# Performance work log

Hardware: AMD Instinct MI355X
Metric: run time of the kernel (lower is better)

## Reference

```python
import jax, jax.numpy as jnp
import numpy as np

B, C, L, D, P = 64, 64, 720, 512, 336
P2, H = P // 2, 512  # H = hidden width of the ProbG branch


def setup_inputs() -> dict:
    key = jax.random.key(0)
    ks = jax.random.split(key, 20)
    def w(k, i, o):
        return jax.random.normal(k, (i, o), jnp.float32) / np.sqrt(i)
    return {
        "x_bsd": jax.random.normal(ks[0], (B, L, C), jnp.float32),
        "z0": jax.random.normal(ks[1], (B, C, D), jnp.float32),
        "y0": jax.random.normal(ks[2], (B, C, P), jnp.float32),
        # ProbG hidden branch (HID_GIVEN_X_V0 -> SS_Z_GIVEN_X_V0)
        "W_h": w(ks[3], L, H),
        "W_ssz": w(ks[4], H, 2 * D),
        # x->z scale/shift flows (versions v2..v5)
        "W_xz_v2": w(ks[5], L, 2 * D),
        "W_xz_v3": w(ks[6], L, 2 * D),
        "W_xz_v4": w(ks[7], L, 2 * D),
        "W_xz_v5": w(ks[8], L, 2 * D),
        # z->x scale/shift flows (v0, v2, v3, v5)
        "W_zx_v0": w(ks[9], D, 2 * L),
        "W_zx_v2": w(ks[10], D, 2 * L),
        "W_zx_v3": w(ks[11], D, 2 * L),
        "W_zx_v5": w(ks[12], D, 2 * L),
        # z->y scale/shift flow (v4, used inside encoding)
        "W_zy_v4": w(ks[13], D, 2 * P),
        # decode heads: ROT_IN_Y_V1 and KOO_Y_GIVEN_Z_V0
        "W_rot": w(ks[14], D, P2),
        "W_koo": w(ks[15], D, 2 * P),
        # Koopman complex params for y-space (a + i b per channel/pair)
        "a_y": jnp.ones((C, P2), jnp.float32),
        "b_y": jnp.zeros((C, P2), jnp.float32) + 0.1,
    }


def _ss(params):
    """Split conditioner output into (positive scale, shift)."""
    s_raw, t = jnp.split(params, 2, axis=-1)
    return jnp.exp(jnp.tanh(s_raw)), t


def _affine(v, cond, W):
    """Scale/shift flow: v <- v * s(cond) + t(cond)."""
    s, t = _ss(jnp.einsum('bck,km->bcm', cond, W))
    return v * s + t


def _rot(u, theta, inv=False):
    """Rotate interleaved (re, im) pairs of u [B,C,P] by angles theta [B,C,P/2]."""
    re, im = u[..., 0::2], u[..., 1::2]
    th = -theta if inv else theta
    c, s = jnp.cos(th), jnp.sin(th)
    return jnp.stack([c * re - s * im, s * re + c * im], axis=-1).reshape(u.shape)


def _koop(u, a, b, inv=False):
    """Koopman unit-complex multiply on interleaved pairs; a,b [C,P/2]."""
    n = jnp.sqrt(a * a + b * b)
    ca, cb = a / n, b / n
    cb = -cb if inv else cb
    re, im = u[..., 0::2], u[..., 1::2]
    return jnp.stack([ca * re - cb * im, cb * re + ca * im], axis=-1).reshape(u.shape)


def reference(x_bsd, z0, y0, W_h, W_ssz, W_xz_v2, W_xz_v3, W_xz_v4, W_xz_v5,
              W_zx_v0, W_zx_v2, W_zx_v3, W_zx_v5, W_zy_v4, W_rot, W_koo, a_y, b_y):
    x = jnp.transpose(x_bsd, (0, 2, 1))  # [B,C,L]
    z = z0 * 0.1                          # [B,C,D]
    y = y0 * 0.1                          # [B,C,P]
    # ---- encoding phase ----
    h = jax.nn.gelu(jnp.einsum('bcl,lk->bck', x, W_h))  # X_to_Z_PROB hidden
    z = _affine(z, h, W_ssz)
    x = _affine(x, z, W_zx_v0)
    z = _affine(z, x, W_xz_v2); x = _affine(x, z, W_zx_v2)
    z = _affine(z, x, W_xz_v3); x = _affine(x, z, W_zx_v3)
    z = _affine(z, x, W_xz_v4); y = _affine(y, z, W_zy_v4)  # Z_to_Y_V4
    z = _affine(z, x, W_xz_v5); x = _affine(x, z, W_zx_v5)
    pre_y = y
    # ---- decode: rotate -> ky -> scale -> ky.inv -> rot.inv -> shift ----
    theta = jnp.pi * jnp.tanh(jnp.einsum('bcd,dp->bcp', z, W_rot))   # [B,C,P/2]
    scale, shift = _ss(jnp.einsum('bcd,dp->bcp', z, W_koo))          # [B,C,P]
    const = _koop(_rot(pre_y, theta), a_y, b_y)
    accu = const * scale
    accu = _rot(_koop(accu, a_y, b_y, inv=True), theta, inv=True) + shift
    return jnp.transpose(accu, (0, 2, 1))  # [B,P,C]
```

## Files before the change

kernel.cpp:

```cpp
#include <hip/hip_runtime.h>
#include <hip/hip_bf16.h>
#include <math.h>

#define BB  64
#define CC  64
#define LL  720
#define LLP 736
#define DD  512
#define PP  336
#define P2C 168
#define HH  512
#define MM  (BB*CC)

typedef _Float16 f16x8 __attribute__((ext_vector_type(8)));
typedef float    f32x4 __attribute__((ext_vector_type(4)));

#define GLDS16(g, l) __builtin_amdgcn_global_load_lds( \
    (const __attribute__((address_space(1))) void*)(g), \
    (__attribute__((address_space(3))) void*)(l), 16, 0, 0)

__device__ __forceinline__ float ftanh(float x) {
  const float ax = fabsf(x);
  const float e  = __expf(2.f * ax);
  const float t  = 1.f - 2.f / (e + 1.f);
  return copysignf(t, x);
}

struct WDesc { const float* src; _Float16* dstHi; _Float16* dstLo;
               int K, N, Kpad, tbase, tilesN; };
struct WTab  { WDesc d[12]; };

__global__ __launch_bounds__(256) void k_convert(WTab tab) {
  __shared__ float tile[16][17];
  const int bid = blockIdx.x;
  int wi = 0;
#pragma unroll
  for (int i = 1; i < 12; ++i) if (bid >= tab.d[i].tbase) wi = i;
  const WDesc d = tab.d[wi];
  const int lt = bid - d.tbase;
  const int tk = lt / d.tilesN, tn = lt % d.tilesN;
  const int k0 = tk * 16, n0 = tn * 16;
  const int tx = threadIdx.x & 15, ty = threadIdx.x >> 4;
  float v = 0.f;
  if (n0 + tx < d.N) v = d.src[(size_t)(k0 + ty) * d.N + n0 + tx];
  tile[ty][tx] = v;
  __syncthreads();
  if (n0 + ty < d.N) {
    const float w = tile[tx][ty];
    const _Float16 h = (_Float16)w;
    const _Float16 l = (_Float16)(w - (float)h);
    const size_t base = (size_t)(n0 + ty) * d.Kpad;
    d.dstHi[base + k0 + tx] = h;
    d.dstLo[base + k0 + tx] = l;
    if (d.Kpad != d.K && k0 + 16 == d.K) {
      d.dstHi[base + d.K + tx] = (_Float16)0.f;
      d.dstLo[base + d.K + tx] = (_Float16)0.f;
    }
  }
}

__global__ __launch_bounds__(256) void k_xpose(const float* __restrict__ xbsd,
                                               _Float16* __restrict__ xhi,
                                               _Float16* __restrict__ xlo) {
  __shared__ float tile[16][17];
  const int b = blockIdx.z, l0 = blockIdx.x * 16, c0 = blockIdx.y * 16;
  const int tx = threadIdx.x, ty = threadIdx.y;
  tile[ty][tx] = xbsd[(size_t)b * LL * CC + (size_t)(l0 + ty) * CC + c0 + tx];
  __syncthreads();
  const float v = tile[tx][ty];
  const _Float16 h = (_Float16)v;
  const _Float16 l = (_Float16)(v - (float)h);
  const size_t m = (size_t)b * CC + c0 + ty;
  xhi[m * LLP + l0 + tx] = h;
  xlo[m * LLP + l0 + tx] = l;
  if (l0 == 704) {
    xhi[m * LLP + 720 + tx] = (_Float16)0.f;
    xlo[m * LLP + 720 + tx] = (_Float16)0.f;
  }
}

template<int EPI, bool DUAL, bool VIN16, bool OUT_T>
__global__ __launch_bounds__(256)
void k_gemm(const _Float16* Ahi, const _Float16* Alo, int lda,
            const _Float16* Whi, const _Float16* Wlo, int ldw,
            const float* Vin32, const _Float16* VinHi,
            const _Float16* VinLo, int ldv, float vscale,
            float* outT32,
            _Float16* outHi, _Float16* outLo, int ldo,
            int Kp, int Nv) {
  constexpr int NB   = DUAL ? 128 : 64;
  constexpr int ABUF = 64 * 32;
  constexpr int BBUF = NB * 32;
  constexpr int SBUF = 2 * ABUF + 2 * BBUF;
  constexpr int NCH  = 8 + 2 * (NB / 16);
  constexpr int NCHW = NCH / 4;
  __shared__ _Float16 smem[2 * SBUF];

  const int gx  = gridDim.x;
  const int nwg = gx * gridDim.y;
  const int id  = blockIdx.y * gx + blockIdx.x;
  const int nid = (id & 7) * (nwg >> 3) + (id >> 3);
  const int m0 = (nid / gx) * 64;
  const int n0 = (nid % gx) * 64;

  {
    const unsigned ph = ((unsigned)nid * 2654435761u) >> 29;
    for (unsigned i = 0; i < ph; ++i) __builtin_amdgcn_s_sleep(8);
  }

  const int tid = threadIdx.x;
  const int w = tid >> 6, lane = tid & 63, q = lane >> 4, r = lane & 15;
  const int wr = (w & 1) * 32, wc = (w >> 1) * 32;
  const int lr = lane >> 2, ls = lane & 3;

  f32x4 accS[2][2] = {};
  f32x4 accT[2][2] = {};

  auto stage = [&](int kc, int bsel) {
    const int k0 = kc << 5;
    _Float16* sb = smem + bsel * SBUF;
#pragma unroll
    for (int cc = 0; cc < NCHW; ++cc) {
      const int chunk = w * NCHW + cc;
      const _Float16* gsrc;
      _Float16* ldst;
      if (chunk < 4) {
        const int rb = chunk * 16;
        const int R = rb + lr;
        const int ss = ls ^ ((R >> 1) & 3);
        gsrc = Ahi + (size_t)(m0 + R) * lda + k0 + ss * 8;
        ldst = sb + rb * 32;
      } else if (chunk < 8) {
        const int rb = (chunk - 4) * 16;
        const int R = rb + lr;
        const int ss = ls ^ ((R >> 1) & 3);
        gsrc = Alo + (size_t)(m0 + R) * lda + k0 + ss * 8;
        ldst = sb + ABUF + rb * 32;
      } else if (chunk < 8 + NB / 16) {
        const int rb = (chunk - 8) * 16;
        const int R = rb + lr;
        const int ss = ls ^ ((R >> 1) & 3);
        const int wrow = (R < 64) ? (n0 + R) : (Nv + n0 + (R - 64));
        gsrc = Whi + (size_t)wrow * ldw + k0 + ss * 8;
        ldst = sb + 2 * ABUF + rb * 32;
      } else {
        const int rb = (chunk - 8 - NB / 16) * 16;
        const int R = rb + lr;
        const int ss = ls ^ ((R >> 1) & 3);
        const int wrow = (R < 64) ? (n0 + R) : (Nv + n0 + (R - 64));
        gsrc = Wlo + (size_t)wrow * ldw + k0 + ss * 8;
        ldst = sb + 2 * ABUF + BBUF + rb * 32;
      }
      GLDS16(gsrc, ldst);
    }
  };

  const int nk = Kp >> 5;
  stage(0, 0);
  int cur = 0;
  for (int kc = 0; kc < nk; ++kc) {
    __syncthreads();
    if (kc + 1 < nk) stage(kc + 1, cur ^ 1);
    const _Float16* sb = smem + cur * SBUF;

    f16x8 ah[2], al[2];
#pragma unroll
    for (int rt = 0; rt < 2; ++rt) {
      const int R = wr + rt * 16 + r;
      const int t = (q ^ ((R >> 1) & 3)) * 8;
      ah[rt] = *(const f16x8*)(sb + R * 32 + t);
      al[rt] = *(const f16x8*)(sb + ABUF + R * 32 + t);
    }
#pragma unroll
    for (int ct = 0; ct < 2; ++ct) {
      const int RB = wc + ct * 16 + r;
      const int tb = (q ^ ((RB >> 1) & 3)) * 8;
      const f16x8 bh = *(const f16x8*)(sb + 2 * ABUF + RB * 32 + tb);
      const f16x8 bl = *(const f16x8*)(sb + 2 * ABUF + BBUF + RB * 32 + tb);
#pragma unroll
      for (int rt = 0; rt < 2; ++rt) {
        accS[rt][ct] = __builtin_amdgcn_mfma_f32_16x16x32_f16(ah[rt], bh, accS[rt][ct], 0, 0, 0);
        accS[rt][ct] = __builtin_amdgcn_mfma_f32_16x16x32_f16(al[rt], bh, accS[rt][ct], 0, 0, 0);
        accS[rt][ct] = __builtin_amdgcn_mfma_f32_16x16x32_f16(ah[rt], bl, accS[rt][ct], 0, 0, 0);
      }
      if (DUAL) {
        const int RT = 64 + RB;
        const int tt = (q ^ ((RT >> 1) & 3)) * 8;
        const f16x8 chh = *(const f16x8*)(sb + 2 * ABUF + RT * 32 + tt);
        const f16x8 cll = *(const f16x8*)(sb + 2 * ABUF + BBUF + RT * 32 + tt);
#pragma unroll
        for (int rt = 0; rt < 2; ++rt) {
          accT[rt][ct] = __builtin_amdgcn_mfma_f32_16x16x32_f16(ah[rt], chh, accT[rt][ct], 0, 0, 0);
          accT[rt][ct] = __builtin_amdgcn_mfma_f32_16x16x32_f16(al[rt], chh, accT[rt][ct], 0, 0, 0);
          accT[rt][ct] = __builtin_amdgcn_mfma_f32_16x16x32_f16(ah[rt], cll, accT[rt][ct], 0, 0, 0);
        }
      }
    }
    cur ^= 1;
  }

#pragma unroll
  for (int rt = 0; rt < 2; ++rt) {
    const int mb = m0 + wr + rt * 16 + q * 4;
#pragma unroll
    for (int ct = 0; ct < 2; ++ct) {
      const int n = n0 + wc + ct * 16 + r;
      if (n >= Nv) continue;
      if (EPI == 2) {
        *(f32x4*)(outT32 + (size_t)n * MM + mb) = accS[rt][ct];
      } else if (EPI == 1) {
#pragma unroll
        for (int g = 0; g < 4; ++g) {
          const int m = mb + g;
          const float v = accS[rt][ct][g];
          const float o = 0.5f * v * (1.0f + ftanh(0.7978845608028654f * (v + 0.044715f * v * v * v)));
          const _Float16 h = (_Float16)o;
          outHi[(size_t)m * ldo + n] = h;
          outLo[(size_t)m * ldo + n] = (_Float16)(o - (float)h);
        }
      } else {
        f32x4 o;
#pragma unroll
        for (int g = 0; g < 4; ++g) {
          const int m = mb + g;
          float v;
          if (VIN16) {
            v = (float)VinHi[(size_t)m * ldv + n] + (float)VinLo[(size_t)m * ldv + n];
          } else {
            v = Vin32[(size_t)m * ldv + n];
          }
          const float s = __expf(ftanh(accS[rt][ct][g]));
          o[g] = v * vscale * s + accT[rt][ct][g];
        }
        if (OUT_T) {
          *(f32x4*)(outT32 + (size_t)n * MM + mb) = o;
        } else {
#pragma unroll
          for (int g = 0; g < 4; ++g) {
            const int m = mb + g;
            const _Float16 h = (_Float16)o[g];
            outHi[(size_t)m * ldo + n] = h;
            outLo[(size_t)m * ldo + n] = (_Float16)(o[g] - (float)h);
          }
        }
      }
    }
  }
}

__global__ __launch_bounds__(256) void k_final(const float* __restrict__ Pt,
                                               const float* __restrict__ yT,
                                               const float* __restrict__ Ay,
                                               const float* __restrict__ By,
                                               float* __restrict__ out) {
  const int c = threadIdx.x;
  const int j = blockIdx.x * 4 + threadIdx.y;
  const int b = blockIdx.y;
  const int m = b * 64 + c;
  const float th = 3.14159265358979323846f * ftanh(Pt[(size_t)j * MM + m]);
  const float sc0 = __expf(ftanh(Pt[(size_t)(168 + 2 * j) * MM + m]));
  const float sc1 = __expf(ftanh(Pt[(size_t)(169 + 2 * j) * MM + m]));
  const float t0 = Pt[(size_t)(504 + 2 * j) * MM + m];
  const float t1 = Pt[(size_t)(505 + 2 * j) * MM + m];
  const float re = yT[(size_t)(2 * j) * MM + m];
  const float im = yT[(size_t)(2 * j + 1) * MM + m];
  const float a = Ay[c * P2C + j], bb = By[c * P2C + j];
  const float rn = rsqrtf(a * a + bb * bb);
  const float ca = a * rn, cb = bb * rn;
  float s1v, c1;
  __sincosf(th, &s1v, &c1);
  const float r1 = c1 * re - s1v * im, i1 = s1v * re + c1 * im;
  const float r2 = ca * r1 - cb * i1,  i2 = cb * r1 + ca * i1;
  const float r3 = r2 * sc0,           i3 = i2 * sc1;
  const float r4 = ca * r3 + cb * i3,  i4 = ca * i3 - cb * r3;
  const float r5 = c1 * r4 + s1v * i4, i5 = c1 * i4 - s1v * r4;
  out[(size_t)b * PP * CC + (size_t)(2 * j) * CC + c]     = r5 + t0;
  out[(size_t)b * PP * CC + (size_t)(2 * j + 1) * CC + c] = i5 + t1;
}

extern "C" void kernel_launch(void* const* d_in, const int* in_sizes, int n_in,
                              void* d_out, int out_size, void* d_ws, size_t ws_size,
                              hipStream_t stream) {
  const float* x_bsd   = (const float*)d_in[0];
  const float* z0      = (const float*)d_in[1];
  const float* y0      = (const float*)d_in[2];
  const float* W_h     = (const float*)d_in[3];
  const float* W_ssz   = (const float*)d_in[4];
  const float* W_xz_v2 = (const float*)d_in[5];
  const float* W_xz_v3 = (const float*)d_in[6];
  const float* W_xz_v4 = (const float*)d_in[7];
  const float* W_xz_v5 = (const float*)d_in[8];
  const float* W_zx_v0 = (const float*)d_in[9];
  const float* W_zx_v2 = (const float*)d_in[10];
  const float* W_zx_v3 = (const float*)d_in[11];
  const float* W_zy_v4 = (const float*)d_in[13];
  const float* W_rot   = (const float*)d_in[14];
  const float* W_koo   = (const float*)d_in[15];
  const float* a_y     = (const float*)d_in[16];
  const float* b_y     = (const float*)d_in[17];
  float* out = (float*)d_out;

  char* p = (char*)d_ws;
  auto alloc = [&](size_t bytes) -> void* {
    void* r = (void*)p; p += (bytes + 255) & ~(size_t)255; return r;
  };
  float*    yT  = (float*)alloc((size_t)PP * MM * 4);
  float*    Pt  = (float*)alloc((size_t)(P2C * 5) * MM * 4);
  _Float16* xhi = (_Float16*)alloc((size_t)MM * LLP * 2);
  _Float16* xlo = (_Float16*)alloc((size_t)MM * LLP * 2);
  _Float16* zhi = (_Float16*)alloc((size_t)MM * DD * 2);
  _Float16* zlo = (_Float16*)alloc((size_t)MM * DD * 2);
  _Float16* hhi = (_Float16*)alloc((size_t)MM * HH * 2);
  _Float16* hlo = (_Float16*)alloc((size_t)MM * HH * 2);
  auto wpair = [&](size_t elems, _Float16** lo) -> _Float16* {
    _Float16* hi = (_Float16*)alloc(elems * 2);
    *lo = (_Float16*)alloc(elems * 2);
    return hi;
  };
  _Float16 *tWhL, *tWsszL, *tWxz2L, *tWxz3L, *tWxz4L, *tWxz5L;
  _Float16 *tWzx0L, *tWzx2L, *tWzx3L, *tWzyL, *tWcatL;
  _Float16* tWh   = wpair((size_t)HH * LLP, &tWhL);
  _Float16* tWssz = wpair((size_t)(2*DD) * DD, &tWsszL);
  _Float16* tWxz2 = wpair((size_t)(2*DD) * LLP, &tWxz2L);
  _Float16* tWxz3 = wpair((size_t)(2*DD) * LLP, &tWxz3L);
  _Float16* tWxz4 = wpair((size_t)(2*DD) * LLP, &tWxz4L);
  _Float16* tWxz5 = wpair((size_t)(2*DD) * LLP, &tWxz5L);
  _Float16* tWzx0 = wpair((size_t)1536 * DD, &tWzx0L);
  _Float16* tWzx2 = wpair((size_t)1536 * DD, &tWzx2L);
  _Float16* tWzx3 = wpair((size_t)1536 * DD, &tWzx3L);
  _Float16* tWzy  = wpair((size_t)768 * DD, &tWzyL);
  _Float16* tWcat = wpair((size_t)896 * DD, &tWcatL);

  WTab tab;
  int base = 0;
  auto put = [&](int i, const float* src, _Float16* dh, _Float16* dl,
                 int K, int N, int Kpad) {
    const int tN = (N + 15) / 16;
    tab.d[i] = WDesc{src, dh, dl, K, N, Kpad, base, tN};
    base += ((K + 15) / 16) * tN;
  };
  put(0,  W_h,     tWh,   tWhL,   LL, HH,   LLP);
  put(1,  W_ssz,   tWssz, tWsszL, DD, 2*DD, DD);
  put(2,  W_xz_v2, tWxz2, tWxz2L, LL, 2*DD, LLP);
  put(3,  W_xz_v3, tWxz3, tWxz3L, LL, 2*DD, LLP);
  put(4,  W_xz_v4, tWxz4, tWxz4L, LL, 2*DD, LLP);
  put(5,  W_xz_v5, tWxz5, tWxz5L, LL, 2*DD, LLP);
  put(6,  W_zx_v0, tWzx0, tWzx0L, DD, 2*LL, DD);
  put(7,  W_zx_v2, tWzx2, tWzx2L, DD, 2*LL, DD);
  put(8,  W_zx_v3, tWzx3, tWzx3L, DD, 2*LL, DD);
  put(9,  W_zy_v4, tWzy,  tWzyL,  DD, 2*PP, DD);
  put(10, W_rot,   tWcat, tWcatL, DD, P2C,  DD);
  put(11, W_koo,   tWcat + (size_t)P2C * DD, tWcatL + (size_t)P2C * DD, DD, 2*PP, DD);
  const int total_tiles = base;

  k_convert<<<dim3(total_tiles), dim3(256), 0, stream>>>(tab);
  k_xpose<<<dim3(45, 4, 64), dim3(16, 16), 0, stream>>>(x_bsd, xhi, xlo);

  const dim3 blk(256);
  k_gemm<1, false, false, false><<<dim3(8, 64), blk, 0, stream>>>(
      xhi, xlo, LLP, tWh, tWhL, LLP,
      nullptr, nullptr, nullptr, 0, 0.f, nullptr, hhi, hlo, HH, LLP, HH);
  k_gemm<0, true, false, false><<<dim3(8, 64), blk, 0, stream>>>(
      hhi, hlo, HH, tWssz, tWsszL, DD,
      z0, nullptr, nullptr, DD, 0.1f, nullptr, zhi, zlo, DD, DD, DD);
  k_gemm<0, true, true, false><<<dim3(12, 64), blk, 0, stream>>>(
      zhi, zlo, DD, tWzx0, tWzx0L, DD,
      nullptr, xhi, xlo, LLP, 1.f, nullptr, xhi, xlo, LLP, DD, LL);
  k_gemm<0, true, true, false><<<dim3(8, 64), blk, 0, stream>>>(
      xhi, xlo, LLP, tWxz2, tWxz2L, LLP,
      nullptr, zhi, zlo, DD, 1.f, nullptr, zhi, zlo, DD, LLP, DD);
  k_gemm<0, true, true, false><<<dim3(12, 64), blk, 0, stream>>>(
      zhi, zlo, DD, tWzx2, tWzx2L, DD,
      nullptr, xhi, xlo, LLP, 1.f, nullptr, xhi, xlo, LLP, DD, LL);
  k_gemm<0, true, true, false><<<dim3(8, 64), blk, 0, stream>>>(
      xhi, xlo, LLP, tWxz3, tWxz3L, LLP,
      nullptr, zhi, zlo, DD, 1.f, nullptr, zhi, zlo, DD, LLP, DD);
  k_gemm<0, true, true, false><<<dim3(12, 64), blk, 0, stream>>>(
      zhi, zlo, DD, tWzx3, tWzx3L, DD,
      nullptr, xhi, xlo, LLP, 1.f, nullptr, xhi, xlo, LLP, DD, LL);
  k_gemm<0, true, true, false><<<dim3(8, 64), blk, 0, stream>>>(
      xhi, xlo, LLP, tWxz4, tWxz4L, LLP,
      nullptr, zhi, zlo, DD, 1.f, nullptr, zhi, zlo, DD, LLP, DD);
  k_gemm<0, true, false, true><<<dim3(6, 64), blk, 0, stream>>>(
      zhi, zlo, DD, tWzy, tWzyL, DD,
      y0, nullptr, nullptr, PP, 0.1f, yT, nullptr, nullptr, 0, DD, PP);
  k_gemm<0, true, true, false><<<dim3(8, 64), blk, 0, stream>>>(
      xhi, xlo, LLP, tWxz5, tWxz5L, LLP,
      nullptr, zhi, zlo, DD, 1.f, nullptr, zhi, zlo, DD, LLP, DD);
  k_gemm<2, false, false, true><<<dim3(14, 64), blk, 0, stream>>>(
      zhi, zlo, DD, tWcat, tWcatL, DD,
      nullptr, nullptr, nullptr, 0, 0.f, Pt, nullptr, nullptr, 0, DD, P2C * 5);
  k_final<<<dim3(42, 64), dim3(64, 4), 0, stream>>>(Pt, yT, a_y, b_y, out);
}
```

Measured before the change: 437.4 us.

## Run independent z->y and x->z v5 GEMMs concurrently in one paired launch

The Z_to_Y_V4 affine and the x->z v5 affine both read z but do not depend on each other. A new grouped kernel runs both in one grid, with the first 512 blocks doing the v5 update and the last 384 doing the y update. The v5 result goes to a new z2 buffer so the y GEMM still reads the old z, and the final GEMM now reads z2. This removes a launch and the tail between the two dependent launches, at the cost of an extra workspace buffer and a random start sleep per block.

```diff
diff --git a/kernel.cpp b/kernel.cpp
--- a/kernel.cpp
+++ b/kernel.cpp
@@ -242,6 +242,162 @@
             outHi[(size_t)m * ldo + n] = h;
             outLo[(size_t)m * ldo + n] = (_Float16)(o[g] - (float)h);
           }
+        }
+      }
+    }
+  }
+}
+
+struct GemmArgs {
+  const _Float16 *Ahi, *Alo; int lda;
+  const _Float16 *Whi, *Wlo; int ldw;
+  const float* Vin32; const _Float16 *VinHi, *VinLo; int ldv; float vscale;
+  float* outT32; _Float16 *outHi, *outLo; int ldo;
+  int Kp, Nv, nblocks, gx;
+};
+
+__global__ __launch_bounds__(256)
+void k_gemm_pair(GemmArgs a0, GemmArgs a1, int split) {
+  constexpr int NB   = 128;
+  constexpr int ABUF = 64 * 32;
+  constexpr int BBUF = NB * 32;
+  constexpr int SBUF = 2 * ABUF + 2 * BBUF;
+  constexpr int NCH  = 8 + 2 * (NB / 16);
+  constexpr int NCHW = NCH / 4;
+  __shared__ _Float16 smem[2 * SBUF];
+
+  const int id = blockIdx.x;
+  const GemmArgs a = (id < split) ? a0 : a1;
+  const int lid = (id < split) ? id : id - split;
+  const int nid = (lid & 7) * (a.nblocks >> 3) + (lid >> 3);
+  const int m0 = (nid / a.gx) * 64;
+  const int n0 = (nid % a.gx) * 64;
+
+  {
+    const unsigned ph = ((unsigned)id * 2654435761u) >> 29;
+    for (unsigned i = 0; i < ph; ++i) __builtin_amdgcn_s_sleep(8);
+  }
+
+  const int tid = threadIdx.x;
+  const int w = tid >> 6, lane = tid & 63, q = lane >> 4, r = lane & 15;
+  const int wr = (w & 1) * 32, wc = (w >> 1) * 32;
+  const int lr = lane >> 2, ls = lane & 3;
+
+  f32x4 accS[2][2] = {};
+  f32x4 accT[2][2] = {};
+
+  auto stage = [&](int kc, int bsel) {
+    const int k0 = kc << 5;
+    _Float16* sb = smem + bsel * SBUF;
+#pragma unroll
+    for (int cc = 0; cc < NCHW; ++cc) {
+      const int chunk = w * NCHW + cc;
+      const _Float16* gsrc;
+      _Float16* ldst;
+      if (chunk < 4) {
+        const int rb = chunk * 16;
+        const int R = rb + lr;
+        const int ss = ls ^ ((R >> 1) & 3);
+        gsrc = a.Ahi + (size_t)(m0 + R) * a.lda + k0 + ss * 8;
+        ldst = sb + rb * 32;
+      } else if (chunk < 8) {
+        const int rb = (chunk - 4) * 16;
+        const int R = rb + lr;
+        const int ss = ls ^ ((R >> 1) & 3);
+        gsrc = a.Alo + (size_t)(m0 + R) * a.lda + k0 + ss * 8;
+        ldst = sb + ABUF + rb * 32;
+      } else if (chunk < 8 + NB / 16) {
+        const int rb = (chunk - 8) * 16;
+        const int R = rb + lr;
+        const int ss = ls ^ ((R >> 1) & 3);
+        const int wrow = (R < 64) ? (n0 + R) : (a.Nv + n0 + (R - 64));
+        gsrc = a.Whi + (size_t)wrow * a.ldw + k0 + ss * 8;
+        ldst = sb + 2 * ABUF + rb * 32;
+      } else {
+        const int rb = (chunk - 8 - NB / 16) * 16;
+        const int R = rb + lr;
+        const int ss = ls ^ ((R >> 1) & 3);
+        const int wrow = (R < 64) ? (n0 + R) : (a.Nv + n0 + (R - 64));
+        gsrc = a.Wlo + (size_t)wrow * a.ldw + k0 + ss * 8;
+        ldst = sb + 2 * ABUF + BBUF + rb * 32;
+      }
+      GLDS16(gsrc, ldst);
+    }
+  };
+
+  const int nk = a.Kp >> 5;
+  stage(0, 0);
+  int cur = 0;
+  for (int kc = 0; kc < nk; ++kc) {
+    __syncthreads();
+    if (kc + 1 < nk) stage(kc + 1, cur ^ 1);
+    const _Float16* sb = smem + cur * SBUF;
+
+    f16x8 ah[2], al[2];
+#pragma unroll
+    for (int rt = 0; rt < 2; ++rt) {
+      const int R = wr + rt * 16 + r;
+      const int t = (q ^ ((R >> 1) & 3)) * 8;
+      ah[rt] = *(const f16x8*)(sb + R * 32 + t);
+      al[rt] = *(const f16x8*)(sb + ABUF + R * 32 + t);
+    }
+#pragma unroll
+    for (int ct = 0; ct < 2; ++ct) {
+      const int RB = wc + ct * 16 + r;
+      const int tb = (q ^ ((RB >> 1) & 3)) * 8;
+      const f16x8 bh = *(const f16x8*)(sb + 2 * ABUF + RB * 32 + tb);
+      const f16x8 bl = *(const f16x8*)(sb + 2 * ABUF + BBUF + RB * 32 + tb);
+#pragma unroll
+      for (int rt = 0; rt < 2; ++rt) {
+        accS[rt][ct] = __builtin_amdgcn_mfma_f32_16x16x32_f16(ah[rt], bh, accS[rt][ct], 0, 0, 0);
+        accS[rt][ct] = __builtin_amdgcn_mfma_f32_16x16x32_f16(al[rt], bh, accS[rt][ct], 0, 0, 0);
+        accS[rt][ct] = __builtin_amdgcn_mfma_f32_16x16x32_f16(ah[rt], bl, accS[rt][ct], 0, 0, 0);
+      }
+      const int RT = 64 + RB;
+      const int tt = (q ^ ((RT >> 1) & 3)) * 8;
+      const f16x8 chh = *(const f16x8*)(sb + 2 * ABUF + RT * 32 + tt);
+      const f16x8 cll = *(const f16x8*)(sb + 2 * ABUF + BBUF + RT * 32 + tt);
+#pragma unroll
+      for (int rt = 0; rt < 2; ++rt) {
+        accT[rt][ct] = __builtin_amdgcn_mfma_f32_16x16x32_f16(ah[rt], chh, accT[rt][ct], 0, 0, 0);
+        accT[rt][ct] = __builtin_amdgcn_mfma_f32_16x16x32_f16(al[rt], chh, accT[rt][ct], 0, 0, 0);
+        accT[rt][ct] = __builtin_amdgcn_mfma_f32_16x16x32_f16(ah[rt], cll, accT[rt][ct], 0, 0, 0);
+      }
+    }
+    cur ^= 1;
+  }
+
+  const bool vin16 = (a.VinHi != nullptr);
+  const bool outT  = (a.outT32 != nullptr);
+#pragma unroll
+  for (int rt = 0; rt < 2; ++rt) {
+    const int mb = m0 + wr + rt * 16 + q * 4;
+#pragma unroll
+    for (int ct = 0; ct < 2; ++ct) {
+      const int n = n0 + wc + ct * 16 + r;
+      if (n >= a.Nv) continue;
+      f32x4 o;
+#pragma unroll
+      for (int g = 0; g < 4; ++g) {
+        const int m = mb + g;
+        float v;
+        if (vin16) {
+          v = (float)a.VinHi[(size_t)m * a.ldv + n] + (float)a.VinLo[(size_t)m * a.ldv + n];
+        } else {
+          v = a.Vin32[(size_t)m * a.ldv + n];
+        }
+        const float s = __expf(ftanh(accS[rt][ct][g]));
+        o[g] = v * a.vscale * s + accT[rt][ct][g];
+      }
+      if (outT) {
+        *(f32x4*)(a.outT32 + (size_t)n * MM + mb) = o;
+      } else {
+#pragma unroll
+        for (int g = 0; g < 4; ++g) {
+          const int m = mb + g;
+          const _Float16 h = (_Float16)o[g];
+          a.outHi[(size_t)m * a.ldo + n] = h;
+          a.outLo[(size_t)m * a.ldo + n] = (_Float16)(o[g] - (float)h);
         }
       }
     }
@@ -310,6 +466,8 @@
   _Float16* xlo = (_Float16*)alloc((size_t)MM * LLP * 2);
   _Float16* zhi = (_Float16*)alloc((size_t)MM * DD * 2);
   _Float16* zlo = (_Float16*)alloc((size_t)MM * DD * 2);
+  _Float16* z2hi = (_Float16*)alloc((size_t)MM * DD * 2);
+  _Float16* z2lo = (_Float16*)alloc((size_t)MM * DD * 2);
   _Float16* hhi = (_Float16*)alloc((size_t)MM * HH * 2);
   _Float16* hlo = (_Float16*)alloc((size_t)MM * HH * 2);
   auto wpair = [&](size_t elems, _Float16** lo) -> _Float16* {
@@ -381,14 +539,22 @@
   k_gemm<0, true, true, false><<<dim3(8, 64), blk, 0, stream>>>(
       xhi, xlo, LLP, tWxz4, tWxz4L, LLP,
       nullptr, zhi, zlo, DD, 1.f, nullptr, zhi, zlo, DD, LLP, DD);
-  k_gemm<0, true, false, true><<<dim3(6, 64), blk, 0, stream>>>(
-      zhi, zlo, DD, tWzy, tWzyL, DD,
-      y0, nullptr, nullptr, PP, 0.1f, yT, nullptr, nullptr, 0, DD, PP);
-  k_gemm<0, true, true, false><<<dim3(8, 64), blk, 0, stream>>>(
-      xhi, xlo, LLP, tWxz5, tWxz5L, LLP,
-      nullptr, zhi, zlo, DD, 1.f, nullptr, zhi, zlo, DD, LLP, DD);
+  {
+    GemmArgs a0, a1;
+    a0.Ahi = xhi;  a0.Alo = xlo;  a0.lda = LLP;
+    a0.Whi = tWxz5; a0.Wlo = tWxz5L; a0.ldw = LLP;
+    a0.Vin32 = nullptr; a0.VinHi = zhi; a0.VinLo = zlo; a0.ldv = DD; a0.vscale = 1.f;
+    a0.outT32 = nullptr; a0.outHi = z2hi; a0.outLo = z2lo; a0.ldo = DD;
+    a0.Kp = LLP; a0.Nv = DD; a0.nblocks = 512; a0.gx = 8;
+    a1.Ahi = zhi;  a1.Alo = zlo;  a1.lda = DD;
+    a1.Whi = tWzy; a1.Wlo = tWzyL; a1.ldw = DD;
+    a1.Vin32 = y0; a1.VinHi = nullptr; a1.VinLo = nullptr; a1.ldv = PP; a1.vscale = 0.1f;
+    a1.outT32 = yT; a1.outHi = nullptr; a1.outLo = nullptr; a1.ldo = 0;
+    a1.Kp = DD; a1.Nv = PP; a1.nblocks = 384; a1.gx = 6;
+    k_gemm_pair<<<dim3(896), blk, 0, stream>>>(a0, a1, 512);
+  }
   k_gemm<2, false, false, true><<<dim3(14, 64), blk, 0, stream>>>(
-      zhi, zlo, DD, tWcat, tWcatL, DD,
+      z2hi, z2lo, DD, tWcat, tWcatL, DD,
       nullptr, nullptr, nullptr, 0, 0.f, Pt, nullptr, nullptr, 0, DD, P2C * 5);
   k_final<<<dim3(42, 64), dim3(64, 4), 0, stream>>>(Pt, yT, a_y, b_y, out);
 }
```

Result: no change. 440.2 us (+0.7%).
